# Kernel optimization log

Hardware: AMD Instinct MI355X
Metric: run time of the kernel (lower is better)

Reference implementation:

```python
import jax, jax.numpy as jnp
import numpy as np

NHEAD = 8
ROUTING_STEPS = 2
TEMP = 1.0
ROPE_THETA = 10000.0


def rmsnorm(x, w, eps=1e-6):
    return x * jax.lax.rsqrt(jnp.mean(x * x, axis=-1, keepdims=True) + eps) * w


def rope_cos_sin(seq_len, head_dim, theta):
    inv = 1.0 / (theta ** (jnp.arange(0, head_dim, 2, dtype=jnp.float32) / head_dim))
    freqs = jnp.outer(jnp.arange(seq_len, dtype=jnp.float32), inv)  # [S, hd/2]
    return jnp.cos(freqs), jnp.sin(freqs)


def apply_rope(x, cos, sin):
    # x: [B,H,S,hd]; cos/sin: [S, hd/2]
    x1, x2 = x[..., 0::2], x[..., 1::2]
    c, s = cos[None, None], sin[None, None]
    r1 = x1 * c - x2 * s
    r2 = x1 * s + x2 * c
    return jnp.stack([r1, r2], axis=-1).reshape(x.shape)


def cube_forward(x, wq, wk, wv, wo, w1, w2, g1, g2, cos, sin):
    # Per-sample gathered expert weights: wq.. [B,D,D], w1 [B,D,F], w2 [B,F,D]
    B, S, D = x.shape
    H = NHEAD
    hd = D // H
    xn = rmsnorm(x, g1[:, None, :])
    q = jnp.einsum('bsd,bde->bse', xn, wq).reshape(B, S, H, hd).transpose(0, 2, 1, 3)
    k = jnp.einsum('bsd,bde->bse', xn, wk).reshape(B, S, H, hd).transpose(0, 2, 1, 3)
    v = jnp.einsum('bsd,bde->bse', xn, wv).reshape(B, S, H, hd).transpose(0, 2, 1, 3)
    q = apply_rope(q, cos, sin)
    k = apply_rope(k, cos, sin)
    scores = jnp.einsum('bhqd,bhkd->bhqk', q, k) / jnp.sqrt(jnp.float32(hd))
    causal = jnp.tril(jnp.ones((S, S), dtype=bool))
    scores = jnp.where(causal, scores, jnp.float32(-1e30))
    att = jax.nn.softmax(scores, axis=-1)
    o = jnp.einsum('bhqk,bhkd->bhqd', att, v).transpose(0, 2, 1, 3).reshape(B, S, D)
    x = x + jnp.einsum('bsd,bde->bse', o, wo)
    hn = rmsnorm(x, g2[:, None, :])
    ff = jax.nn.silu(jnp.einsum('bsd,bdf->bsf', hn, w1))
    return x + jnp.einsum('bsf,bfd->bsd', ff, w2)


def reference(input_ids, start_cubes, emb, Wq, Wk, Wv, Wo, W1, W2, n1, n2, gate_w, final_norm_w, fc_out_w):
    B, S = input_ids.shape
    D = emb.shape[1]
    C = Wq.shape[0]
    x = emb[input_ids] * jnp.sqrt(jnp.float32(D))
    cos, sin = rope_cos_sin(S, D // NHEAD, ROPE_THETA)
    # deterministic ring graph: neighbors of cube i are (i+1)%C and (i+2)%C
    ar = jnp.arange(C)
    adj = jnp.zeros((C, C), dtype=bool).at[ar, (ar + 1) % C].set(True).at[ar, (ar + 2) % C].set(True)
    cur = start_cubes
    acc_probs = jnp.zeros(C + 1, dtype=jnp.float32)
    acc_lb = jnp.float32(0.0)
    for _ in range(ROUTING_STEPS):
        x = cube_forward(x, Wq[cur], Wk[cur], Wv[cur], Wo[cur], W1[cur], W2[cur], n1[cur], n2[cur], cos, sin)
        pooled = x.mean(axis=1)                        # [B, D]
        scores = pooled @ gate_w                       # [B, C+1]
        probs = jax.nn.softmax(scores / TEMP, axis=-1)
        acc_probs = acc_probs + probs.sum(axis=0)
        avg = probs.mean(axis=0)
        acc_lb = acc_lb + (C + 1) * jnp.sum(avg * avg)
        masked = jnp.where(adj[cur], scores[:, :C], jnp.float32(-1e30))
        cur = jnp.argmax(masked, axis=-1)
    logits = jnp.einsum('bsd,dv->bsv', rmsnorm(x, final_norm_w), fc_out_w)
    avg_probs = acc_probs / jnp.float32(ROUTING_STEPS * B)
    aux_variance_loss = jnp.var(avg_probs)
    aux_lb_loss = acc_lb / jnp.float32(ROUTING_STEPS)
    return logits, aux_variance_loss, aux_lb_loss


def setup_inputs() -> dict:
    key = jax.random.key(0)
    ks = jax.random.split(key, 16)
    V, D, F, C, B, S = 32000, 512, 2048, 4, 2, 256
    w = 0.02
    return {
        'input_ids': jax.random.randint(ks[0], (B, S), 0, V),
        'start_cubes': jax.random.randint(ks[1], (B,), 0, C),
        'emb': jax.random.normal(ks[2], (V, D), jnp.float32) * w,
        'Wq': jax.random.normal(ks[3], (C, D, D), jnp.float32) * w,
        'Wk': jax.random.normal(ks[4], (C, D, D), jnp.float32) * w,
        'Wv': jax.random.normal(ks[5], (C, D, D), jnp.float32) * w,
        'Wo': jax.random.normal(ks[6], (C, D, D), jnp.float32) * w,
        'W1': jax.random.normal(ks[7], (C, D, F), jnp.float32) * w,
        'W2': jax.random.normal(ks[8], (C, F, D), jnp.float32) * w,
        'n1': jnp.ones((C, D), jnp.float32),
        'n2': jnp.ones((C, D), jnp.float32),
        'gate_w': jax.random.normal(ks[9], (D, C + 1), jnp.float32) * w,
        'final_norm_w': jnp.ones((D,), jnp.float32),
        'fc_out_w': jax.random.normal(ks[10], (D, V), jnp.float32) * w,
    }
```

## Files before the change

### kernel.cpp

```cpp
#include <hip/hip_runtime.h>
#include <hip/hip_bf16.h>

#define BB 2
#define SS 256
#define DDIM 512
#define HH 8
#define HDIM 64
#define FDIM 2048
#define CC 4
#define VV 32000
#define NTOK (BB*SS)
#define PCHUNK 16

typedef __hip_bfloat16 bf16;
typedef __attribute__((ext_vector_type(8))) short short8;
typedef __attribute__((ext_vector_type(4))) short short4v;
typedef __attribute__((ext_vector_type(4))) float floatx4;

__device__ __forceinline__ int get_mode(const unsigned* __restrict__ probe) {
    return (probe[0] == 0x3F800000u) ? 0 : 1;
}
__device__ __forceinline__ float ldw(const void* __restrict__ p, long i, int mode) {
    if (mode == 0) return ((const float*)p)[i];
    return __bfloat162float(((const bf16*)p)[i]);
}
__device__ __forceinline__ void stf(void* __restrict__ p, long i, float v, int mode) {
    if (mode == 0) ((float*)p)[i] = v;
    else ((bf16*)p)[i] = __float2bfloat16(v);
}

__global__ void init_kernel(const int* __restrict__ ids,
                            const int* __restrict__ start_cubes,
                            const void* __restrict__ emb,
                            float* __restrict__ x,
                            float* __restrict__ acc_probs,
                            float* __restrict__ acc_lb,
                            int* __restrict__ cur,
                            const unsigned* __restrict__ probe) {
    int mode = get_mode(probe);
    int gid = blockIdx.x * blockDim.x + threadIdx.x;
    if (gid < NTOK * DDIM) {
        int tok = gid / DDIM, d = gid % DDIM;
        x[gid] = ldw(emb, (long)ids[tok] * DDIM + d, mode) * 22.627416997969522f;
    }
    if (gid < CC + 1) acc_probs[gid] = 0.f;
    if (gid == CC + 1) *acc_lb = 0.f;
    if (gid < BB) cur[gid] = start_cubes[gid];
}

__global__ void rmsnorm_kernel(const float* __restrict__ in,
                               void* __restrict__ out, int obf,
                               const void* __restrict__ gamma,
                               const int* __restrict__ cur,
                               float* __restrict__ zbuf, int zn,
                               const unsigned* __restrict__ probe) {
    int mode = get_mode(probe);
    int tok = blockIdx.x;
    int b = tok / SS;
    long goff = cur ? (long)cur[b] * DDIM : 0;
    if (zbuf) {
        int gtid = blockIdx.x * blockDim.x + threadIdx.x;
        int gstride = gridDim.x * blockDim.x;
        for (int i = gtid; i < zn; i += gstride) zbuf[i] = 0.f;
    }
    __shared__ float red[256];
    int t = threadIdx.x;
    float x0 = in[(long)tok * DDIM + t];
    float x1 = in[(long)tok * DDIM + t + 256];
    red[t] = x0 * x0 + x1 * x1;
    __syncthreads();
    for (int s = 128; s > 0; s >>= 1) {
        if (t < s) red[t] += red[t + s];
        __syncthreads();
    }
    float scale = rsqrtf(red[0] / DDIM + 1e-6f);
    float v0 = x0 * scale * ldw(gamma, goff + t, mode);
    float v1 = x1 * scale * ldw(gamma, goff + t + 256, mode);
    if (obf) {
        ((bf16*)out)[(long)tok * DDIM + t]       = __float2bfloat16(v0);
        ((bf16*)out)[(long)tok * DDIM + t + 256] = __float2bfloat16(v1);
    } else {
        ((float*)out)[(long)tok * DDIM + t]       = v0;
        ((float*)out)[(long)tok * DDIM + t + 256] = v1;
    }
}

__global__ void silu_kernel(const float* __restrict__ in,
                            ushort* __restrict__ out, int n) {
    int i4 = (blockIdx.x * blockDim.x + threadIdx.x) * 4;
    if (i4 >= n) return;
    float4 v = *(const float4*)&in[i4];
    float a = v.x / (1.f + expf(-v.x));
    float b = v.y / (1.f + expf(-v.y));
    float c = v.z / (1.f + expf(-v.z));
    float d = v.w / (1.f + expf(-v.w));
    bf16 t0 = __float2bfloat16(a), t1 = __float2bfloat16(b);
    bf16 t2 = __float2bfloat16(c), t3 = __float2bfloat16(d);
    short4v o;
    o[0] = *(short*)&t0; o[1] = *(short*)&t1;
    o[2] = *(short*)&t2; o[3] = *(short*)&t3;
    *(short4v*)&out[i4] = o;
}

__global__ void transpose_kernel(const void* __restrict__ in, bf16* __restrict__ out,
                                 int K, int N, long ims, long oms,
                                 const unsigned* __restrict__ probe) {
    int mode = get_mode(probe);
    __shared__ float tile[32][33];
    int mat = blockIdx.z;
    int n0 = blockIdx.x * 32, k0 = blockIdx.y * 32;
    int tx = threadIdx.x, ty = threadIdx.y;
#pragma unroll
    for (int i = 0; i < 4; i++)
        tile[ty + i * 8][tx] = ldw(in, (long)mat * ims + (long)(k0 + ty + i * 8) * N + (n0 + tx), mode);
    __syncthreads();
#pragma unroll
    for (int i = 0; i < 4; i++)
        out[(long)mat * oms + (long)(n0 + ty + i * 8) * K + (k0 + tx)] =
            __float2bfloat16(tile[tx][ty + i * 8]);
}

__global__ __launch_bounds__(256)
void gemm_mfma(const ushort* __restrict__ A,
               const ushort* __restrict__ WtB,
               const int* __restrict__ cur, long wcube, long wz,
               int K, int N,
               const float* __restrict__ res,
               void* __restrict__ out, long ozstride,
               int omode, int ACT, int nsplit,
               const unsigned* __restrict__ probe) {
    int mode = get_mode(probe);
    __shared__ __align__(16) ushort sA[128 * 40];
    __shared__ __align__(16) ushort sB[128 * 40];
    int tid = threadIdx.x;
    int m0 = blockIdx.y * 128;
    int n0 = blockIdx.x * 128;
    int z  = blockIdx.z / nsplit;
    int ks = blockIdx.z % nsplit;
    int Kc = K / nsplit;
    int kbeg = ks * Kc, kend = kbeg + Kc;
    const ushort* Wt = WtB + (long)z * wz + (cur ? (long)cur[m0 / SS] * wcube : 0);
    floatx4 acc[4][4];
#pragma unroll
    for (int i = 0; i < 4; i++)
#pragma unroll
        for (int j = 0; j < 4; j++)
#pragma unroll
            for (int r = 0; r < 4; r++) acc[i][j][r] = 0.f;
    int w = tid >> 6, lane = tid & 63;
    int wm = (w & 1) * 64, wn = (w >> 1) * 64;
    int lr = lane & 15, quad = lane >> 4;

    for (int k0 = kbeg; k0 < kend; k0 += 32) {
        __syncthreads();
#pragma unroll
        for (int i = 0; i < 2; i++) {
            int g = tid + i * 256;
            int r = g >> 2, c8 = (g & 3) * 8;
            *(short8*)&sA[r * 40 + c8] = *(const short8*)&A[(long)(m0 + r) * K + k0 + c8];
            *(short8*)&sB[r * 40 + c8] = *(const short8*)&Wt[(long)(n0 + r) * K + k0 + c8];
        }
        __syncthreads();
        short8 af[4], bfr[4];
#pragma unroll
        for (int i = 0; i < 4; i++) {
            af[i]  = *(const short8*)&sA[(wm + i * 16 + lr) * 40 + quad * 8];
            bfr[i] = *(const short8*)&sB[(wn + i * 16 + lr) * 40 + quad * 8];
        }
#pragma unroll
        for (int mi = 0; mi < 4; mi++)
#pragma unroll
            for (int ni = 0; ni < 4; ni++)
                acc[mi][ni] = __builtin_amdgcn_mfma_f32_16x16x32_bf16(af[mi], bfr[ni], acc[mi][ni], 0, 0, 0);
    }
#pragma unroll
    for (int mi = 0; mi < 4; mi++)
#pragma unroll
        for (int ni = 0; ni < 4; ni++) {
            int col = n0 + wn + ni * 16 + lr;
#pragma unroll
            for (int r = 0; r < 4; r++) {
                int row = m0 + wm + mi * 16 + quad * 4 + r;
                float v = acc[mi][ni][r];
                long oi = (long)z * ozstride + (long)row * N + col;
                if (omode == 3) {
                    atomicAdd((float*)out + oi, v);
                } else {
                    if (ACT == 1) v = v / (1.f + expf(-v));
                    if (res) v += res[(long)row * N + col];
                    if (omode == 0)      ((float*)out)[oi] = v;
                    else if (omode == 1) ((bf16*)out)[oi] = __float2bfloat16(v);
                    else                 stf(out, oi, v, mode);
                }
            }
        }
}

__global__ void rope_kernel(float* __restrict__ q, float* __restrict__ k) {
    int gid = blockIdx.x * blockDim.x + threadIdx.x;
    if (gid >= NTOK * HH * (HDIM / 2)) return;
    int j = gid % (HDIM / 2);
    int rest = gid / (HDIM / 2);
    int h = rest % HH;
    int tok = rest / HH;
    int s = tok % SS;
    float inv = expf(-(float)j * (logf(10000.f) / 32.f));
    float ang = (float)s * inv;
    float c = cosf(ang), sn = sinf(ang);
    long base = (long)tok * DDIM + h * HDIM + 2 * j;
    float q1 = q[base], q2 = q[base + 1];
    q[base]     = q1 * c - q2 * sn;
    q[base + 1] = q1 * sn + q2 * c;
    float k1 = k[base], k2 = k[base + 1];
    k[base]     = k1 * c - k2 * sn;
    k[base + 1] = k1 * sn + k2 * c;
}

__global__ void attn_kernel(const float* __restrict__ q,
                            const float* __restrict__ k,
                            const float* __restrict__ v,
                            void* __restrict__ o, int obf) {
    int blk = blockIdx.x;
    int qr = blk % SS;
    int h = (blk / SS) % HH;
    int b = blk / (SS * HH);
    int t = threadIdx.x;
    __shared__ float sc[256];
    __shared__ float red[256];
    __shared__ float qs[HDIM];
    long qbase = ((long)(b * SS + qr)) * DDIM + h * HDIM;
    if (t < HDIM) qs[t] = q[qbase + t];
    __syncthreads();
    float s = -1e30f;
    if (t <= qr) {
        long kbase = ((long)(b * SS + t)) * DDIM + h * HDIM;
        float acc = 0.f;
#pragma unroll
        for (int i = 0; i < HDIM; i++) acc += qs[i] * k[kbase + i];
        s = acc * 0.125f;
    }
    sc[t] = s;
    red[t] = s;
    __syncthreads();
    for (int st = 128; st > 0; st >>= 1) {
        if (t < st) red[t] = fmaxf(red[t], red[t + st]);
        __syncthreads();
    }
    float m = red[0];
    __syncthreads();
    float e = (t <= qr) ? expf(sc[t] - m) : 0.f;
    sc[t] = e;
    red[t] = e;
    __syncthreads();
    for (int st = 128; st > 0; st >>= 1) {
        if (t < st) red[t] += red[t + st];
        __syncthreads();
    }
    float invsum = 1.f / red[0];
    if (t < HDIM) {
        float acc = 0.f;
        for (int kk = 0; kk <= qr; kk++)
            acc += sc[kk] * v[((long)(b * SS + kk)) * DDIM + h * HDIM + t];
        float vv = acc * invsum;
        if (obf) ((bf16*)o)[qbase + t] = __float2bfloat16(vv);
        else     ((float*)o)[qbase + t] = vv;
    }
}

__global__ void pool_partial_kernel(const float* __restrict__ x,
                                    float* __restrict__ partial) {
    int blk = blockIdx.x;
    int b = blk / (SS / PCHUNK);
    int c = blk % (SS / PCHUNK);
    int t = threadIdx.x;
    float acc = 0.f;
    long base = ((long)b * SS + c * PCHUNK) * DDIM + t;
#pragma unroll
    for (int i = 0; i < PCHUNK; i++) acc += x[base + (long)i * DDIM];
    partial[(long)blk * DDIM + t] = acc;
}

__global__ void routing_kernel(const float* __restrict__ partial,
                               const void* __restrict__ gate_w,
                               float* __restrict__ acc_probs,
                               float* __restrict__ acc_lb,
                               int* __restrict__ cur,
                               int final_step,
                               void* __restrict__ d_out,
                               const unsigned* __restrict__ probe) {
    int mode = get_mode(probe);
    __shared__ float pooled[BB][DDIM];
    __shared__ float scores[BB][CC + 1];
    int t = threadIdx.x;
#pragma unroll
    for (int b = 0; b < BB; b++) {
        float acc = 0.f;
#pragma unroll
        for (int c = 0; c < SS / PCHUNK; c++)
            acc += partial[((long)b * (SS / PCHUNK) + c) * DDIM + t];
        pooled[b][t] = acc / (float)SS;
    }
    __syncthreads();
    if (t < BB * (CC + 1)) {
        int b = t / (CC + 1), c = t % (CC + 1);
        float acc = 0.f;
        for (int d = 0; d < DDIM; d++)
            acc += pooled[b][d] * ldw(gate_w, (long)d * (CC + 1) + c, mode);
        scores[b][c] = acc;
    }
    __syncthreads();
    if (t == 0) {
        float probs[BB][CC + 1];
        for (int b = 0; b < BB; b++) {
            float m = -1e30f;
            for (int c = 0; c <= CC; c++) m = fmaxf(m, scores[b][c]);
            float sum = 0.f;
            for (int c = 0; c <= CC; c++) { probs[b][c] = expf(scores[b][c] - m); sum += probs[b][c]; }
            for (int c = 0; c <= CC; c++) probs[b][c] /= sum;
        }
        float lb = 0.f;
        for (int c = 0; c <= CC; c++) {
            float sumb = 0.f;
            for (int b = 0; b < BB; b++) sumb += probs[b][c];
            acc_probs[c] += sumb;
            float avg = sumb / (float)BB;
            lb += avg * avg;
        }
        *acc_lb += (float)(CC + 1) * lb;
        for (int b = 0; b < BB; b++) {
            int cu = cur[b];
            int a1 = (cu + 1) % CC, a2 = (cu + 2) % CC;
            float best = -1e38f; int bi = 0;
            for (int c = 0; c < CC; c++) {
                float vv = (c == a1 || c == a2) ? scores[b][c] : -1e30f;
                if (vv > best) { best = vv; bi = c; }
            }
            cur[b] = bi;
        }
        if (final_step) {
            float ap[CC + 1], mean = 0.f;
            for (int c = 0; c <= CC; c++) { ap[c] = acc_probs[c] / (2.f * BB); mean += ap[c]; }
            mean /= (float)(CC + 1);
            float var = 0.f;
            for (int c = 0; c <= CC; c++) { float d = ap[c] - mean; var += d * d; }
            var /= (float)(CC + 1);
            stf(d_out, (long)NTOK * VV + 0, var, mode);
            stf(d_out, (long)NTOK * VV + 1, (*acc_lb) / 2.f, mode);
        }
    }
}

template <int TM, int ACT, bool OUT_DYN>
__global__ void gemm_kernel(const float* __restrict__ A,
                            const void* __restrict__ Wbase,
                            const int* __restrict__ cur, long wstride,
                            int K, int N,
                            const float* __restrict__ res,
                            void* __restrict__ out,
                            const unsigned* __restrict__ probe) {
    int mode = get_mode(probe);
    extern __shared__ float sA[];
    int row0 = blockIdx.y * TM;
    long woff = cur ? (long)cur[row0 / SS] * wstride : 0;
    int t = threadIdx.x;
    for (int i = t; i < TM * K; i += 256)
        sA[i] = A[(long)(row0 + i / K) * K + (i % K)];
    __syncthreads();
    int n = blockIdx.x * 256 + t;
    float acc[TM];
#pragma unroll
    for (int r = 0; r < TM; r++) acc[r] = 0.f;
    for (int k = 0; k < K; k++) {
        float w = ldw(Wbase, woff + (long)k * N + n, mode);
#pragma unroll
        for (int r = 0; r < TM; r++) acc[r] += sA[r * K + k] * w;
    }
#pragma unroll
    for (int r = 0; r < TM; r++) {
        float v = acc[r];
        if (ACT == 1) v = v / (1.f + expf(-v));
        if (res) v += res[(long)(row0 + r) * N + n];
        long oi = (long)(row0 + r) * N + n;
        if constexpr (OUT_DYN) stf(out, oi, v, mode);
        else                   ((float*)out)[oi] = v;
    }
}

__global__ void routing_kernel_fb(const float* __restrict__ x,
                                  const void* __restrict__ gate_w,
                                  float* __restrict__ acc_probs,
                                  float* __restrict__ acc_lb,
                                  int* __restrict__ cur,
                                  int final_step,
                                  void* __restrict__ d_out,
                                  const unsigned* __restrict__ probe) {
    int mode = get_mode(probe);
    __shared__ float pooled[BB][DDIM];
    __shared__ float scores[BB][CC + 1];
    int t = threadIdx.x;
    for (int b = 0; b < BB; b++) {
        float acc = 0.f;
        for (int s = 0; s < SS; s++) acc += x[((long)(b * SS + s)) * DDIM + t];
        pooled[b][t] = acc / (float)SS;
    }
    __syncthreads();
    if (t < BB * (CC + 1)) {
        int b = t / (CC + 1), c = t % (CC + 1);
        float acc = 0.f;
        for (int d = 0; d < DDIM; d++)
            acc += pooled[b][d] * ldw(gate_w, (long)d * (CC + 1) + c, mode);
        scores[b][c] = acc;
    }
    __syncthreads();
    if (t == 0) {
        float probs[BB][CC + 1];
        for (int b = 0; b < BB; b++) {
            float m = -1e30f;
            for (int c = 0; c <= CC; c++) m = fmaxf(m, scores[b][c]);
            float sum = 0.f;
            for (int c = 0; c <= CC; c++) { probs[b][c] = expf(scores[b][c] - m); sum += probs[b][c]; }
            for (int c = 0; c <= CC; c++) probs[b][c] /= sum;
        }
        float lb = 0.f;
        for (int c = 0; c <= CC; c++) {
            float sumb = 0.f;
            for (int b = 0; b < BB; b++) sumb += probs[b][c];
            acc_probs[c] += sumb;
            float avg = sumb / (float)BB;
            lb += avg * avg;
        }
        *acc_lb += (float)(CC + 1) * lb;
        for (int b = 0; b < BB; b++) {
            int cu = cur[b];
            int a1 = (cu + 1) % CC, a2 = (cu + 2) % CC;
            float best = -1e38f; int bi = 0;
            for (int c = 0; c < CC; c++) {
                float vv = (c == a1 || c == a2) ? scores[b][c] : -1e30f;
                if (vv > best) { best = vv; bi = c; }
            }
            cur[b] = bi;
        }
        if (final_step) {
            float ap[CC + 1], mean = 0.f;
            for (int c = 0; c <= CC; c++) { ap[c] = acc_probs[c] / (2.f * BB); mean += ap[c]; }
            mean /= (float)(CC + 1);
            float var = 0.f;
            for (int c = 0; c <= CC; c++) { float d = ap[c] - mean; var += d * d; }
            var /= (float)(CC + 1);
            stf(d_out, (long)NTOK * VV + 0, var, mode);
            stf(d_out, (long)NTOK * VV + 1, (*acc_lb) / 2.f, mode);
        }
    }
}

extern "C" void kernel_launch(void* const* d_in, const int* in_sizes, int n_in,
                              void* d_out, int out_size, void* d_ws, size_t ws_size,
                              hipStream_t stream) {
    const int*  ids   = (const int*)d_in[0];
    const int*  start = (const int*)d_in[1];
    const void* emb   = d_in[2];
    const void* Wq    = d_in[3];
    const void* Wk    = d_in[4];
    const void* Wv    = d_in[5];
    const void* Wo    = d_in[6];
    const void* W1    = d_in[7];
    const void* W2    = d_in[8];
    const void* n1    = d_in[9];
    const void* n2    = d_in[10];
    const void* gate  = d_in[11];
    const void* fnorm = d_in[12];
    const void* fcw   = d_in[13];
    const unsigned* probe = (const unsigned*)d_in[9];

    char* base = (char*)d_ws;
    size_t off = 0;
    auto alloc = [&](size_t bytes) { size_t p = off; off = (off + bytes + 255) & ~(size_t)255; return p; };
    size_t x_o    = alloc((size_t)NTOK * DDIM * 4);
    size_t qkv_o  = alloc((size_t)3 * NTOK * DDIM * 4);
    size_t xn_o   = alloc((size_t)NTOK * DDIM * 2);
    size_t ob_o   = alloc((size_t)NTOK * DDIM * 2);
    size_t ff_o   = alloc((size_t)NTOK * FDIM * 2);
    size_t ffp_o  = alloc((size_t)NTOK * FDIM * 4);
    size_t acc_o  = alloc(256);
    size_t part_o = alloc((size_t)BB * (SS / PCHUNK) * DDIM * 4);
    size_t qkvT_o = alloc((size_t)3 * CC * DDIM * DDIM * 2);
    size_t WoT_o  = alloc((size_t)CC * DDIM * DDIM * 2);
    size_t W1T_o  = alloc((size_t)CC * DDIM * FDIM * 2);
    size_t W2T_o  = alloc((size_t)CC * FDIM * DDIM * 2);
    size_t fcwT_o = alloc((size_t)DDIM * VV * 2);
    bool big = ws_size >= off;

    if (big) {
        float* x    = (float*)(base + x_o);
        float* qkv  = (float*)(base + qkv_o);
        float* q = qkv, *k = qkv + NTOK * DDIM, *v = qkv + 2 * NTOK * DDIM;
        bf16*  xn   = (bf16*)(base + xn_o);
        bf16*  ob   = (bf16*)(base + ob_o);
        bf16*  ff   = (bf16*)(base + ff_o);
        float* ffp  = (float*)(base + ffp_o);
        float* acc_probs = (float*)(base + acc_o);
        float* acc_lb = acc_probs + 8;
        int*   cur = (int*)(acc_lb + 8);
        float* partial = (float*)(base + part_o);
        bf16* qkvT = (bf16*)(base + qkvT_o);
        bf16* WoT  = (bf16*)(base + WoT_o);
        bf16* W1T  = (bf16*)(base + W1T_o);
        bf16* W2T  = (bf16*)(base + W2T_o);
        bf16* fcwT = (bf16*)(base + fcwT_o);

        dim3 tb(32, 8);
        transpose_kernel<<<dim3(16, 16, CC), tb, 0, stream>>>(Wq, qkvT,                 DDIM, DDIM, (long)DDIM*DDIM, (long)DDIM*DDIM, probe);
        transpose_kernel<<<dim3(16, 16, CC), tb, 0, stream>>>(Wk, qkvT +   CC*DDIM*DDIM, DDIM, DDIM, (long)DDIM*DDIM, (long)DDIM*DDIM, probe);
        transpose_kernel<<<dim3(16, 16, CC), tb, 0, stream>>>(Wv, qkvT + 2*CC*DDIM*DDIM, DDIM, DDIM, (long)DDIM*DDIM, (long)DDIM*DDIM, probe);
        transpose_kernel<<<dim3(16, 16, CC), tb, 0, stream>>>(Wo, WoT,  DDIM, DDIM, (long)DDIM*DDIM, (long)DDIM*DDIM, probe);
        transpose_kernel<<<dim3(64, 16, CC), tb, 0, stream>>>(W1, W1T,  DDIM, FDIM, (long)DDIM*FDIM, (long)FDIM*DDIM, probe);
        transpose_kernel<<<dim3(16, 64, CC), tb, 0, stream>>>(W2, W2T,  FDIM, DDIM, (long)FDIM*DDIM, (long)DDIM*FDIM, probe);
        transpose_kernel<<<dim3(1000, 16, 1), tb, 0, stream>>>(fcw, fcwT, DDIM, VV, 0, 0, probe);

        init_kernel<<<(NTOK * DDIM + 255) / 256, 256, 0, stream>>>(
            ids, start, emb, x, acc_probs, acc_lb, cur, probe);

        const long DD2 = (long)DDIM * DDIM;
        const int QS = 4;
        const int OS = 4;
        const int F1S = 4;
        const int F2S = 8;
        for (int step = 0; step < 2; step++) {
            rmsnorm_kernel<<<NTOK, 256, 0, stream>>>(x, xn, 1, n1, cur,
                                                     qkv, 3 * NTOK * DDIM, probe);
            gemm_mfma<<<dim3(DDIM/128, NTOK/128, 3*QS), 256, 0, stream>>>(
                (const ushort*)xn, (const ushort*)qkvT, cur, DD2, (long)CC*DD2,
                DDIM, DDIM, nullptr, qkv, (long)NTOK*DDIM, 3, 0, QS, probe);
            rope_kernel<<<(NTOK * HH * (HDIM / 2) + 255) / 256, 256, 0, stream>>>(q, k);
            attn_kernel<<<BB * HH * SS, 256, 0, stream>>>(q, k, v, ob, 1);
            gemm_mfma<<<dim3(DDIM/128, NTOK/128, OS), 256, 0, stream>>>(
                (const ushort*)ob, (const ushort*)WoT, cur, DD2, 0,
                DDIM, DDIM, nullptr, x, 0, 3, 0, OS, probe);
            rmsnorm_kernel<<<NTOK, 256, 0, stream>>>(x, xn, 1, n2, cur,
                                                     ffp, NTOK * FDIM, probe);
            gemm_mfma<<<dim3(FDIM/128, NTOK/128, F1S), 256, 0, stream>>>(
                (const ushort*)xn, (const ushort*)W1T, cur, (long)FDIM*DDIM, 0,
                DDIM, FDIM, nullptr, ffp, 0, 3, 0, F1S, probe);
            silu_kernel<<<(NTOK * FDIM / 4 + 255) / 256, 256, 0, stream>>>(
                ffp, (ushort*)ff, NTOK * FDIM);
            gemm_mfma<<<dim3(DDIM/128, NTOK/128, F2S), 256, 0, stream>>>(
                (const ushort*)ff, (const ushort*)W2T, cur, (long)DDIM*FDIM, 0,
                FDIM, DDIM, nullptr, x, 0, 3, 0, F2S, probe);
            pool_partial_kernel<<<BB * (SS / PCHUNK), 512, 0, stream>>>(x, partial);
            routing_kernel<<<1, 512, 0, stream>>>(
                partial, gate, acc_probs, acc_lb, cur, step == 1, d_out, probe);
        }
        rmsnorm_kernel<<<NTOK, 256, 0, stream>>>(x, xn, 1, fnorm, nullptr,
                                                 nullptr, 0, probe);
        gemm_mfma<<<dim3(VV/128, NTOK/128, 1), 256, 0, stream>>>(
            (const ushort*)xn, (const ushort*)fcwT, nullptr, 0, 0,
            DDIM, VV, nullptr, d_out, 0, 2, 0, 1, probe);
        return;
    }

    float* ws = (float*)d_ws;
    float* x  = ws;
    float* xn = x  + NTOK * DDIM;
    float* q  = xn + NTOK * DDIM;
    float* k  = q  + NTOK * DDIM;
    float* v  = k  + NTOK * DDIM;
    float* o  = v  + NTOK * DDIM;
    float* ff = o  + NTOK * DDIM;
    float* acc_probs = ff + NTOK * FDIM;
    float* acc_lb    = acc_probs + 8;
    int*   cur       = (int*)(acc_lb + 8);
    const long DD2 = (long)DDIM * DDIM;

    init_kernel<<<(NTOK * DDIM + 255) / 256, 256, 0, stream>>>(
        ids, start, emb, x, acc_probs, acc_lb, cur, probe);
    for (int step = 0; step < 2; step++) {
        rmsnorm_kernel<<<NTOK, 256, 0, stream>>>(x, xn, 0, n1, cur, nullptr, 0, probe);
        dim3 gdd(DDIM / 256, NTOK / 16);
        size_t smem16 = 16 * DDIM * sizeof(float);
        gemm_kernel<16, 0, false><<<gdd, 256, smem16, stream>>>(
            xn, Wq, cur, DD2, DDIM, DDIM, nullptr, q, probe);
        gemm_kernel<16, 0, false><<<gdd, 256, smem16, stream>>>(
            xn, Wk, cur, DD2, DDIM, DDIM, nullptr, k, probe);
        gemm_kernel<16, 0, false><<<gdd, 256, smem16, stream>>>(
            xn, Wv, cur, DD2, DDIM, DDIM, nullptr, v, probe);
        rope_kernel<<<(NTOK * HH * (HDIM / 2) + 255) / 256, 256, 0, stream>>>(q, k);
        attn_kernel<<<BB * HH * SS, 256, 0, stream>>>(q, k, v, o, 0);
        gemm_kernel<16, 0, false><<<gdd, 256, smem16, stream>>>(
            o, Wo, cur, DD2, DDIM, DDIM, x, x, probe);
        rmsnorm_kernel<<<NTOK, 256, 0, stream>>>(x, xn, 0, n2, cur, nullptr, 0, probe);
        dim3 gdf(FDIM / 256, NTOK / 16);
        gemm_kernel<16, 1, false><<<gdf, 256, smem16, stream>>>(
            xn, W1, cur, (long)DDIM * FDIM, DDIM, FDIM, nullptr, ff, probe);
        dim3 gfd(DDIM / 256, NTOK / 4);
        size_t smem4f = 4 * FDIM * sizeof(float);
        gemm_kernel<4, 0, false><<<gfd, 256, smem4f, stream>>>(
            ff, W2, cur, (long)FDIM * DDIM, FDIM, DDIM, x, x, probe);
        routing_kernel_fb<<<1, 512, 0, stream>>>(
            x, gate, acc_probs, acc_lb, cur, step == 1, d_out, probe);
    }
    rmsnorm_kernel<<<NTOK, 256, 0, stream>>>(x, xn, 0, fnorm, nullptr, nullptr, 0, probe);
    dim3 gv(VV / 256, NTOK / 16);
    size_t smem16 = 16 * DDIM * sizeof(float);
    gemm_kernel<16, 0, true><<<gv, 256, smem16, stream>>>(
        xn, fcw, nullptr, 0, DDIM, VV, nullptr, d_out, probe);
}
```

Before: 586.7 us.

## Use direct global-to-LDS loads in GEMM, XCD tile swizzle, and parallelize attention PV

The GEMM tile loads now use global_load_lds to copy 16-byte chunks straight into shared memory, and the padded LDS row stride is dropped so the layout matches the load order. An optional block-index swizzle groups tiles per XCD and is switched on only for the large vocabulary projection, to improve L2 reuse of the weight columns. The attention P·V loop is split across all 256 threads in four key groups and reduced in shared memory, where before only 64 threads did the work. Removing the padding can bring back LDS bank conflicts on the fragment reads, and the swizzle assumes the tile count divides evenly by 8.

```diff
diff --git a/kernel.cpp b/kernel.cpp
--- a/kernel.cpp
+++ b/kernel.cpp
@@ -27,6 +27,12 @@
 __device__ __forceinline__ void stf(void* __restrict__ p, long i, float v, int mode) {
     if (mode == 0) ((float*)p)[i] = v;
     else ((bf16*)p)[i] = __float2bfloat16(v);
+}
+
+__device__ __forceinline__ void gload16(const void* g, void* l) {
+    __builtin_amdgcn_global_load_lds(
+        (const __attribute__((address_space(1))) unsigned int*)g,
+        (__attribute__((address_space(3))) unsigned int*)l, 16, 0, 0);
 }
 
 __global__ void init_kernel(const int* __restrict__ ids,
@@ -127,14 +133,25 @@
                int K, int N,
                const float* __restrict__ res,
                void* __restrict__ out, long ozstride,
-               int omode, int ACT, int nsplit,
+               int omode, int ACT, int nsplit, int swz,
                const unsigned* __restrict__ probe) {
     int mode = get_mode(probe);
-    __shared__ __align__(16) ushort sA[128 * 40];
-    __shared__ __align__(16) ushort sB[128 * 40];
+    __shared__ __align__(16) ushort sA[128 * 32];
+    __shared__ __align__(16) ushort sB[128 * 32];
     int tid = threadIdx.x;
-    int m0 = blockIdx.y * 128;
-    int n0 = blockIdx.x * 128;
+    int mi = blockIdx.y, ni = blockIdx.x;
+    if (swz) {
+        int nb = gridDim.x, mb = gridDim.y;
+        int lin = blockIdx.x + blockIdx.y * nb;
+        int nwg = nb * mb;
+        int q = nwg >> 3;
+        int xcd = lin & 7, pos = lin >> 3;
+        int nid = xcd * q + pos;
+        mi = nid % mb;
+        ni = nid / mb;
+    }
+    int m0 = mi * 128;
+    int n0 = ni * 128;
     int z  = blockIdx.z / nsplit;
     int ks = blockIdx.z % nsplit;
     int Kc = K / nsplit;
@@ -157,31 +174,31 @@
         for (int i = 0; i < 2; i++) {
             int g = tid + i * 256;
             int r = g >> 2, c8 = (g & 3) * 8;
-            *(short8*)&sA[r * 40 + c8] = *(const short8*)&A[(long)(m0 + r) * K + k0 + c8];
-            *(short8*)&sB[r * 40 + c8] = *(const short8*)&Wt[(long)(n0 + r) * K + k0 + c8];
+            gload16(&A[(long)(m0 + r) * K + k0 + c8],  &sA[g * 8]);
+            gload16(&Wt[(long)(n0 + r) * K + k0 + c8], &sB[g * 8]);
         }
         __syncthreads();
         short8 af[4], bfr[4];
 #pragma unroll
         for (int i = 0; i < 4; i++) {
-            af[i]  = *(const short8*)&sA[(wm + i * 16 + lr) * 40 + quad * 8];
-            bfr[i] = *(const short8*)&sB[(wn + i * 16 + lr) * 40 + quad * 8];
-        }
-#pragma unroll
-        for (int mi = 0; mi < 4; mi++)
-#pragma unroll
-            for (int ni = 0; ni < 4; ni++)
-                acc[mi][ni] = __builtin_amdgcn_mfma_f32_16x16x32_bf16(af[mi], bfr[ni], acc[mi][ni], 0, 0, 0);
-    }
-#pragma unroll
-    for (int mi = 0; mi < 4; mi++)
-#pragma unroll
-        for (int ni = 0; ni < 4; ni++) {
-            int col = n0 + wn + ni * 16 + lr;
+            af[i]  = *(const short8*)&sA[(wm + i * 16 + lr) * 32 + quad * 8];
+            bfr[i] = *(const short8*)&sB[(wn + i * 16 + lr) * 32 + quad * 8];
+        }
+#pragma unroll
+        for (int mm = 0; mm < 4; mm++)
+#pragma unroll
+            for (int nn = 0; nn < 4; nn++)
+                acc[mm][nn] = __builtin_amdgcn_mfma_f32_16x16x32_bf16(af[mm], bfr[nn], acc[mm][nn], 0, 0, 0);
+    }
+#pragma unroll
+    for (int mm = 0; mm < 4; mm++)
+#pragma unroll
+        for (int nn = 0; nn < 4; nn++) {
+            int col = n0 + wn + nn * 16 + lr;
 #pragma unroll
             for (int r = 0; r < 4; r++) {
-                int row = m0 + wm + mi * 16 + quad * 4 + r;
-                float v = acc[mi][ni][r];
+                int row = m0 + wm + mm * 16 + quad * 4 + r;
+                float v = acc[mm][nn][r];
                 long oi = (long)z * ozstride + (long)row * N + col;
                 if (omode == 3) {
                     atomicAdd((float*)out + oi, v);
@@ -257,11 +274,15 @@
         __syncthreads();
     }
     float invsum = 1.f / red[0];
+    __syncthreads();
+    int g = t >> 6, d = t & 63;
+    float pacc = 0.f;
+    for (int kk = g; kk <= qr; kk += 4)
+        pacc += sc[kk] * v[((long)(b * SS + kk)) * DDIM + h * HDIM + d];
+    red[t] = pacc;
+    __syncthreads();
     if (t < HDIM) {
-        float acc = 0.f;
-        for (int kk = 0; kk <= qr; kk++)
-            acc += sc[kk] * v[((long)(b * SS + kk)) * DDIM + h * HDIM + t];
-        float vv = acc * invsum;
+        float vv = (red[t] + red[t + 64] + red[t + 128] + red[t + 192]) * invsum;
         if (obf) ((bf16*)o)[qbase + t] = __float2bfloat16(vv);
         else     ((float*)o)[qbase + t] = vv;
     }
@@ -530,22 +551,22 @@
                                                      qkv, 3 * NTOK * DDIM, probe);
             gemm_mfma<<<dim3(DDIM/128, NTOK/128, 3*QS), 256, 0, stream>>>(
                 (const ushort*)xn, (const ushort*)qkvT, cur, DD2, (long)CC*DD2,
-                DDIM, DDIM, nullptr, qkv, (long)NTOK*DDIM, 3, 0, QS, probe);
+                DDIM, DDIM, nullptr, qkv, (long)NTOK*DDIM, 3, 0, QS, 0, probe);
             rope_kernel<<<(NTOK * HH * (HDIM / 2) + 255) / 256, 256, 0, stream>>>(q, k);
             attn_kernel<<<BB * HH * SS, 256, 0, stream>>>(q, k, v, ob, 1);
             gemm_mfma<<<dim3(DDIM/128, NTOK/128, OS), 256, 0, stream>>>(
                 (const ushort*)ob, (const ushort*)WoT, cur, DD2, 0,
-                DDIM, DDIM, nullptr, x, 0, 3, 0, OS, probe);
+                DDIM, DDIM, nullptr, x, 0, 3, 0, OS, 0, probe);
             rmsnorm_kernel<<<NTOK, 256, 0, stream>>>(x, xn, 1, n2, cur,
                                                      ffp, NTOK * FDIM, probe);
             gemm_mfma<<<dim3(FDIM/128, NTOK/128, F1S), 256, 0, stream>>>(
                 (const ushort*)xn, (const ushort*)W1T, cur, (long)FDIM*DDIM, 0,
-                DDIM, FDIM, nullptr, ffp, 0, 3, 0, F1S, probe);
+                DDIM, FDIM, nullptr, ffp, 0, 3, 0, F1S, 0, probe);
             silu_kernel<<<(NTOK * FDIM / 4 + 255) / 256, 256, 0, stream>>>(
                 ffp, (ushort*)ff, NTOK * FDIM);
             gemm_mfma<<<dim3(DDIM/128, NTOK/128, F2S), 256, 0, stream>>>(
                 (const ushort*)ff, (const ushort*)W2T, cur, (long)DDIM*FDIM, 0,
-                FDIM, DDIM, nullptr, x, 0, 3, 0, F2S, probe);
+                FDIM, DDIM, nullptr, x, 0, 3, 0, F2S, 0, probe);
             pool_partial_kernel<<<BB * (SS / PCHUNK), 512, 0, stream>>>(x, partial);
             routing_kernel<<<1, 512, 0, stream>>>(
                 partial, gate, acc_probs, acc_lb, cur, step == 1, d_out, probe);
@@ -554,7 +575,7 @@
                                                  nullptr, 0, probe);
         gemm_mfma<<<dim3(VV/128, NTOK/128, 1), 256, 0, stream>>>(
             (const ushort*)xn, (const ushort*)fcwT, nullptr, 0, 0,
-            DDIM, VV, nullptr, d_out, 0, 2, 0, 1, probe);
+            DDIM, VV, nullptr, d_out, 0, 2, 0, 1, 1, probe);
         return;
     }
 
```

Result: no change. 596.6 us (+1.7%).
